# Kernel optimization log

Hardware: AMD Instinct MI355X
Metric: run time of the kernel (lower is better)

Reference implementation:

```python
import jax, jax.numpy as jnp
import numpy as np

HEIGHT = 8  # init kwarg: output crop height
B, J, C, HIMG, WIMG = 8, 64, 32, 256, 256


def _make_boxes():
    rng = np.random.default_rng(0)
    left = rng.uniform(0.0, 40.0, (B, J))
    bw = rng.uniform(16.0, 200.0, (B, J))
    top = rng.uniform(0.0, 200.0, (B, J))
    bh = rng.uniform(8.0, 32.0, (B, J))
    theta = rng.uniform(-0.5, 0.5, (B, J))  # unused by the original forward
    return np.stack([left, top, left + bw, top + bh, theta], axis=-1).astype(np.float32)


def _box_widths(boxes_np):
    # torch: width = int(aspect * height), truncation (values are positive)
    bw = boxes_np[..., 2] - boxes_np[..., 0]
    bh = boxes_np[..., 3] - boxes_np[..., 1]
    return ((bw / bh) * HEIGHT).astype(np.int32)  # [B, J]


def setup_inputs() -> dict:
    key = jax.random.key(0)
    image = jax.random.normal(key, (B, C, HIMG, WIMG), dtype=jnp.float32)
    boxes = jnp.asarray(_make_boxes())
    return {"image": image, "boxes": boxes}


def reference(image, boxes):
    # Per-box widths are integer (shape-determining) constants, taken from concrete box data.
    boxes_np = np.asarray(jax.device_get(boxes))
    widths_np = _box_widths(boxes_np)          # [B, J] ints >= 2
    max_w = int(widths_np.max())
    widths = jnp.asarray(widths_np)

    dt = boxes.dtype
    base_w = boxes[..., 2] - boxes[..., 0]      # [B, J]
    base_h = boxes[..., 3] - boxes[..., 1]
    each_w = base_w / (widths.astype(dt) - 1)   # [B, J]
    each_h = base_h / (HEIGHT - 1)

    # Sampling grids: xx [B,J,Wm], yy [B,J,Hh]
    xx = jnp.arange(max_w, dtype=dt)[None, None, :] * each_w[..., None] + boxes[..., 0:1]
    yy = jnp.arange(HEIGHT, dtype=dt)[None, None, :] * each_h[..., None] + boxes[..., 1:2]

    def interp_one_image(img, x, y):
        # img [C,Hi,Wi], x [J,Wm], y [J,Hh] -> [C,J,Hh,Wm]
        x0 = jnp.clip(jnp.floor(x).astype(jnp.int32), 0, WIMG - 1)
        x1 = jnp.clip(jnp.floor(x).astype(jnp.int32) + 1, 0, WIMG - 1)
        y0 = jnp.clip(jnp.floor(y).astype(jnp.int32), 0, HIMG - 1)
        y1 = jnp.clip(jnp.floor(y).astype(jnp.int32) + 1, 0, HIMG - 1)
        # gathers: [C, J, Hh, Wm]
        ia = img[:, y0[:, :, None], x0[:, None, :]]
        ib = img[:, y1[:, :, None], x0[:, None, :]]
        ic = img[:, y0[:, :, None], x1[:, None, :]]
        idd = img[:, y1[:, :, None], x1[:, None, :]]
        x0f, x1f = x0.astype(dt), x1.astype(dt)
        y0f, y1f = y0.astype(dt), y1.astype(dt)
        wa = (x1f - x)[:, None, :] * (y1f - y)[:, :, None]  # [J,Hh,Wm]
        wb = (x1f - x)[:, None, :] * (y - y0f)[:, :, None]
        wc = (x - x0f)[:, None, :] * (y1f - y)[:, :, None]
        wd = (x - x0f)[:, None, :] * (y - y0f)[:, :, None]
        return ia * wa[None] + ib * wb[None] + ic * wc[None] + idd * wd[None]

    res = jax.vmap(interp_one_image)(image, xx, yy)      # [B,C,J,Hh,Wm]
    res = jnp.transpose(res, (0, 2, 1, 3, 4))            # [B,J,C,Hh,Wm]

    mask = (jnp.arange(max_w)[None, None, :] < widths[..., None]).astype(jnp.uint8)  # [B,J,Wm]
    res = res * mask[:, :, None, None, :].astype(res.dtype)  # zero-pad beyond each box width
    return res, mask
```

## Files before the change

### kernel.cpp

```cpp
#include <hip/hip_runtime.h>

#define HIMG 256
#define WIMG 256
#define CCH  32
#define JBOX 64
#define BIMG 8
#define HGT  8
#define CPB  8
#define NCG  (CCH / CPB)
#define NXCD 8
#define LSEG 208
#define LPAD 216

__global__ __launch_bounds__(256, 6) void roi_kernel(
    const float* __restrict__ img,
    const float* __restrict__ boxes,
    float* __restrict__ res,
    float* __restrict__ mask,
    int max_w)
{
    __shared__ float sblend[CPB][LPAD];

    const int d    = blockIdx.x;
    const int slot = d & (NXCD - 1);
    const int seq  = d >> 3;
    const int bj   = slot * ((BIMG * JBOX) / NXCD) + (seq >> 5);
    const int rem  = seq & 31;
    const int h    = rem >> 2;
    const int cg   = rem & 3;
    const int b    = bj >> 6;
    const int tid  = threadIdx.x;

    const float left = boxes[bj * 5 + 0];
    const float top  = boxes[bj * 5 + 1];
    const float bw   = boxes[bj * 5 + 2] - left;
    const float bh   = boxes[bj * 5 + 3] - top;

    const int   width  = (int)(bw / bh * 8.0f);
    const float each_w = bw / ((float)width - 1.0f);
    const float each_h = bh / 7.0f;

    const float y  = __fadd_rn(__fmul_rn((float)h, each_h), top);
    const int   yf = (int)floorf(y);
    const int   y0 = min(max(yf,     0), HIMG - 1);
    const int   y1 = min(max(yf + 1, 0), HIMG - 1);
    const float wy1 = (float)y1 - y;
    const float wy0 = y - (float)y0;

    const int xs  = max((int)floorf(left), 0);
    const int xs4 = xs & ~3;

    {
        const float* base = img + ((size_t)b * CCH + cg * CPB) * (HIMG * WIMG);
        #pragma unroll
        for (int it = 0; it < 2; ++it) {
            const int item = it * 256 + tid;
            const int ch   = item >> 6;
            const int l    = item & 63;
            if (l < 52) {
                const float* r0p = base + ((size_t)ch * HIMG + y0) * WIMG + xs4 + l * 4;
                const float* r1p = base + ((size_t)ch * HIMG + y1) * WIMG + xs4 + l * 4;
                const float4 q0 = *reinterpret_cast<const float4*>(r0p);
                const float4 q1 = *reinterpret_cast<const float4*>(r1p);
                const float b0 = q0.x * wy1 + q1.x * wy0;
                const float b1 = q0.y * wy1 + q1.y * wy0;
                const float b2 = q0.z * wy1 + q1.z * wy0;
                const float b3 = q0.w * wy1 + q1.w * wy0;
                const int c = l * 4;
                const int p = c + (c >> 5);
                float* wp = &sblend[ch][p];
                wp[0] = b0;
                wp[1] = b1;
                wp[2] = b2;
                wp[3] = b3;
                if ((l & 7) == 0 && l != 0) {
                    wp[-1] = b0;
                }
            }
        }
    }

    __syncthreads();

    const int  i    = tid;
    const bool have = (i < max_w);
    const bool in_w = (i < width);

    if (h == 0 && cg == 0 && have) {
        mask[(size_t)bj * max_w + i] = in_w ? 1.0f : 0.0f;
    }

    float* resp = res + (((size_t)bj * CCH + cg * CPB) * HGT + h) * (size_t)max_w + i;
    const size_t c_stride = (size_t)HGT * max_w;

    if (!have) return;

    if (!in_w) {
        #pragma unroll
        for (int c = 0; c < CPB; ++c) {
            resp[(size_t)c * c_stride] = 0.0f;
        }
        return;
    }

    const float x  = __fadd_rn(__fmul_rn((float)i, each_w), left);
    const int   xf = (int)floorf(x);
    const int   x0 = min(max(xf, 0), WIMG - 1);
    const float wx1 = (float)(x0 + 1) - x;
    const float wx0 = x - (float)x0;

    const int lx0 = min(max(x0 - xs4, 0), LSEG - 2);
    const int p0  = lx0 + (lx0 >> 5);

    const float* rp = &sblend[0][p0];
    #pragma unroll
    for (int c = 0; c < CPB; ++c) {
        const float v0 = rp[0];
        const float v1 = rp[1];
        resp[(size_t)c * c_stride] = v0 * wx1 + v1 * wx0;
        rp += LPAD;
    }
}

extern "C" void kernel_launch(void* const* d_in, const int* in_sizes, int n_in,
                              void* d_out, int out_size, void* d_ws, size_t ws_size,
                              hipStream_t stream) {
    const float* img   = (const float*)d_in[0];
    const float* boxes = (const float*)d_in[1];
    float* out = (float*)d_out;

    const int per_w = BIMG * JBOX * CCH * HGT + BIMG * JBOX;
    const int max_w = out_size / per_w;

    float* res  = out;
    float* mask = out + (size_t)BIMG * JBOX * CCH * HGT * max_w;

    const int blocks = BIMG * JBOX * HGT * NCG;
    roi_kernel<<<blocks, 256, 0, stream>>>(img, boxes, res, mask, max_w);
}
```

Measured before the change: 151.0 us.

## Loop over crop rows inside each block with double-buffered LDS and load prefetch

Each block now processes all 8 output rows for one (box, channel-group) instead of one row, which cuts the grid by a factor of 8. The next row's global loads are issued before the barrier and the current row's horizontal interpolation, and a double-buffered shared array overlaps blend writes with reads. This is meant to hide global-load latency and amortize per-block setup, at the cost of fewer blocks (2048) and a longer serial loop per block. The occupancy hint rises to 8.

```diff
diff --git a/kernel.cpp b/kernel.cpp
--- a/kernel.cpp
+++ b/kernel.cpp
@@ -12,22 +12,20 @@
 #define LSEG 208
 #define LPAD 216
 
-__global__ __launch_bounds__(256, 6) void roi_kernel(
+__global__ __launch_bounds__(256, 8) void roi_kernel(
     const float* __restrict__ img,
     const float* __restrict__ boxes,
     float* __restrict__ res,
     float* __restrict__ mask,
     int max_w)
 {
-    __shared__ float sblend[CPB][LPAD];
+    __shared__ float sblend[2][CPB][LPAD];
 
     const int d    = blockIdx.x;
     const int slot = d & (NXCD - 1);
     const int seq  = d >> 3;
-    const int bj   = slot * ((BIMG * JBOX) / NXCD) + (seq >> 5);
-    const int rem  = seq & 31;
-    const int h    = rem >> 2;
-    const int cg   = rem & 3;
+    const int bj   = slot * ((BIMG * JBOX) / NXCD) + (seq >> 2);
+    const int cg   = seq & 3;
     const int b    = bj >> 6;
     const int tid  = threadIdx.x;
 
@@ -40,85 +38,108 @@
     const float each_w = bw / ((float)width - 1.0f);
     const float each_h = bh / 7.0f;
 
-    const float y  = __fadd_rn(__fmul_rn((float)h, each_h), top);
-    const int   yf = (int)floorf(y);
-    const int   y0 = min(max(yf,     0), HIMG - 1);
-    const int   y1 = min(max(yf + 1, 0), HIMG - 1);
-    const float wy1 = (float)y1 - y;
-    const float wy0 = y - (float)y0;
-
     const int xs  = max((int)floorf(left), 0);
     const int xs4 = xs & ~3;
-
-    {
-        const float* base = img + ((size_t)b * CCH + cg * CPB) * (HIMG * WIMG);
-        #pragma unroll
-        for (int it = 0; it < 2; ++it) {
-            const int item = it * 256 + tid;
-            const int ch   = item >> 6;
-            const int l    = item & 63;
-            if (l < 52) {
-                const float* r0p = base + ((size_t)ch * HIMG + y0) * WIMG + xs4 + l * 4;
-                const float* r1p = base + ((size_t)ch * HIMG + y1) * WIMG + xs4 + l * 4;
-                const float4 q0 = *reinterpret_cast<const float4*>(r0p);
-                const float4 q1 = *reinterpret_cast<const float4*>(r1p);
-                const float b0 = q0.x * wy1 + q1.x * wy0;
-                const float b1 = q0.y * wy1 + q1.y * wy0;
-                const float b2 = q0.z * wy1 + q1.z * wy0;
-                const float b3 = q0.w * wy1 + q1.w * wy0;
-                const int c = l * 4;
-                const int p = c + (c >> 5);
-                float* wp = &sblend[ch][p];
-                wp[0] = b0;
-                wp[1] = b1;
-                wp[2] = b2;
-                wp[3] = b3;
-                if ((l & 7) == 0 && l != 0) {
-                    wp[-1] = b0;
-                }
-            }
-        }
-    }
-
-    __syncthreads();
 
     const int  i    = tid;
     const bool have = (i < max_w);
     const bool in_w = (i < width);
-
-    if (h == 0 && cg == 0 && have) {
-        mask[(size_t)bj * max_w + i] = in_w ? 1.0f : 0.0f;
-    }
-
-    float* resp = res + (((size_t)bj * CCH + cg * CPB) * HGT + h) * (size_t)max_w + i;
-    const size_t c_stride = (size_t)HGT * max_w;
-
-    if (!have) return;
-
-    if (!in_w) {
-        #pragma unroll
-        for (int c = 0; c < CPB; ++c) {
-            resp[(size_t)c * c_stride] = 0.0f;
-        }
-        return;
-    }
-
     const float x  = __fadd_rn(__fmul_rn((float)i, each_w), left);
     const int   xf = (int)floorf(x);
     const int   x0 = min(max(xf, 0), WIMG - 1);
     const float wx1 = (float)(x0 + 1) - x;
     const float wx0 = x - (float)x0;
-
     const int lx0 = min(max(x0 - xs4, 0), LSEG - 2);
     const int p0  = lx0 + (lx0 >> 5);
 
-    const float* rp = &sblend[0][p0];
+    if (cg == 0 && have) {
+        mask[(size_t)bj * max_w + i] = in_w ? 1.0f : 0.0f;
+    }
+
+    const int  l   = tid & 63;
+    const bool act = (l < 52);
+    const int  chA = tid >> 6;
+    const int  chB = chA + 4;
+    const int  coloff = xs4 + l * 4;
+    const float* base = img + ((size_t)b * CCH + cg * CPB) * (HIMG * WIMG);
+    const float* rowA = base + (size_t)chA * (HIMG * WIMG) + coloff;
+    const float* rowB = base + (size_t)chB * (HIMG * WIMG) + coloff;
+
+    const int  c   = l * 4;
+    const int  pw  = c + (c >> 5);
+    const bool hole = act && ((l & 7) == 0) && (l != 0);
+
+    const size_t c_stride = (size_t)HGT * max_w;
+    float* resp0 = res + (((size_t)bj * CCH + cg * CPB) * HGT) * (size_t)max_w + i;
+
+    int y0n, y1n; float wy0n, wy1n;
+    auto taps = [&](int h) {
+        const float y  = __fadd_rn(__fmul_rn((float)h, each_h), top);
+        const int   yf = (int)floorf(y);
+        y0n = min(max(yf,     0), HIMG - 1);
+        y1n = min(max(yf + 1, 0), HIMG - 1);
+        wy1n = (float)y1n - y;
+        wy0n = y - (float)y0n;
+    };
+
+    float4 qA0, qA1, qB0, qB1;
+    auto issue = [&](int y0, int y1) {
+        if (act) {
+            qA0 = *reinterpret_cast<const float4*>(rowA + (size_t)y0 * WIMG);
+            qA1 = *reinterpret_cast<const float4*>(rowA + (size_t)y1 * WIMG);
+            qB0 = *reinterpret_cast<const float4*>(rowB + (size_t)y0 * WIMG);
+            qB1 = *reinterpret_cast<const float4*>(rowB + (size_t)y1 * WIMG);
+        }
+    };
+
+    taps(0);
+    issue(y0n, y1n);
+    float w0c = wy0n, w1c = wy1n;
+
     #pragma unroll
-    for (int c = 0; c < CPB; ++c) {
-        const float v0 = rp[0];
-        const float v1 = rp[1];
-        resp[(size_t)c * c_stride] = v0 * wx1 + v1 * wx0;
-        rp += LPAD;
+    for (int h = 0; h < HGT; ++h) {
+        const int buf = h & 1;
+
+        if (act) {
+            const float a0 = qA0.x * w1c + qA1.x * w0c;
+            const float a1 = qA0.y * w1c + qA1.y * w0c;
+            const float a2 = qA0.z * w1c + qA1.z * w0c;
+            const float a3 = qA0.w * w1c + qA1.w * w0c;
+            float* wp = &sblend[buf][chA][pw];
+            wp[0] = a0; wp[1] = a1; wp[2] = a2; wp[3] = a3;
+            if (hole) wp[-1] = a0;
+            const float b0 = qB0.x * w1c + qB1.x * w0c;
+            const float b1 = qB0.y * w1c + qB1.y * w0c;
+            const float b2 = qB0.z * w1c + qB1.z * w0c;
+            const float b3 = qB0.w * w1c + qB1.w * w0c;
+            float* wq = &sblend[buf][chB][pw];
+            wq[0] = b0; wq[1] = b1; wq[2] = b2; wq[3] = b3;
+            if (hole) wq[-1] = b0;
+        }
+
+        if (h < HGT - 1) {
+            taps(h + 1);
+            issue(y0n, y1n);
+        }
+
+        asm volatile("s_waitcnt lgkmcnt(0)" ::: "memory");
+        __builtin_amdgcn_s_barrier();
+        __builtin_amdgcn_sched_barrier(0);
+
+        if (have) {
+            float* resp = resp0 + (size_t)h * max_w;
+            const float* rp = &sblend[buf][0][p0];
+            #pragma unroll
+            for (int cc = 0; cc < CPB; ++cc) {
+                const float v0 = rp[0];
+                const float v1 = rp[1];
+                const float val = v0 * wx1 + v1 * wx0;
+                resp[(size_t)cc * c_stride] = in_w ? val : 0.0f;
+                rp += LPAD;
+            }
+        }
+
+        w0c = wy0n; w1c = wy1n;
     }
 }
 
@@ -135,6 +156,6 @@
     float* res  = out;
     float* mask = out + (size_t)BIMG * JBOX * CCH * HGT * max_w;
 
-    const int blocks = BIMG * JBOX * HGT * NCG;
+    const int blocks = BIMG * JBOX * NCG;
     roi_kernel<<<blocks, 256, 0, stream>>>(img, boxes, res, mask, max_w);
 }
```

After: 156.3 us. +3.5%, slower.
